# Kernel tuning notes

Measured on AMD Instinct MI355X. Metric: run time of the kernel, lower is better.

The kernel has to match this reference:

```python
import jax, jax.numpy as jnp
import numpy as np

B, S, F, H = 16, 2048, 1024, 16
D = F // H
EPS = 1e-5


def setup_inputs() -> dict:
    key = jax.random.key(0)
    ks = jax.random.split(key, 10)
    scale = 1.0 / np.sqrt(F)
    return {
        "x": jax.random.normal(ks[0], (B, S, F), jnp.float32),
        "Wq": jax.random.normal(ks[1], (F, F), jnp.float32) * scale,
        "bq": jnp.zeros((F,), jnp.float32),
        "Wk": jax.random.normal(ks[2], (F, F), jnp.float32) * scale,
        "bk": jnp.zeros((F,), jnp.float32),
        "Wv": jax.random.normal(ks[3], (F, F), jnp.float32) * scale,
        "bv": jnp.zeros((F,), jnp.float32),
        "Wo": jax.random.normal(ks[4], (F, F), jnp.float32) * scale,
        "bo": jnp.zeros((F,), jnp.float32),
        "gamma": jnp.ones((F,), jnp.float32),
        "beta": jnp.zeros((F,), jnp.float32),
    }


def reference(x, Wq, bq, Wk, bk, Wv, bv, Wo, bo, gamma, beta):
    # x: (B, S, F). Dropout is identity in eval mode.
    b, s, f = x.shape
    q = (x @ Wq + bq).reshape(b, s, H, D)
    k = (x @ Wk + bk).reshape(b, s, H, D)
    v = (x @ Wv + bv).reshape(b, s, H, D)
    # Faithful to source: the einsum (applied to permuted tensors) contracts
    # across HEADS at each sequence position -> scores (B, S, H, H).
    energy = jnp.einsum('bshd,bsgd->bshg', q, k) / (D ** 0.5)
    attn = jax.nn.softmax(energy, axis=-1)  # softmax over key-head axis
    out = jnp.einsum('bshg,bsgd->bshd', attn, v).reshape(b, s, f)
    out = out @ Wo + bo
    # LayerNorm over last dim (eps=1e-5, affine)
    mu = jnp.mean(out, axis=-1, keepdims=True)
    var = jnp.mean((out - mu) ** 2, axis=-1, keepdims=True)
    return (out - mu) * jax.lax.rsqrt(var + EPS) * gamma + beta
```

## Files before the change

kernel.cpp:

```cpp
#include <hip/hip_runtime.h>
#include <hip/hip_bf16.h>
#include <stdint.h>

#define MM   32768
#define FFD  1024
#define NQKV 3072

typedef __bf16 bf16x8 __attribute__((ext_vector_type(8)));
typedef float  f32x4  __attribute__((ext_vector_type(4)));

__device__ __forceinline__ unsigned short f2bf_bits(float f){
  __hip_bfloat16 h = __float2bfloat16(f);
  unsigned short u;
  __builtin_memcpy(&u, &h, 2);
  return u;
}

__device__ __forceinline__ float bf2f(unsigned short u){
  unsigned int w = ((unsigned int)u) << 16;
  float f;
  __builtin_memcpy(&f, &w, 4);
  return f;
}

__device__ __forceinline__ void gld16(const void* g, void* l){
  const unsigned int* gu = (const unsigned int*)g;
  unsigned int* lu = (unsigned int*)l;
  __builtin_amdgcn_global_load_lds(
      (const __attribute__((address_space(1))) unsigned int*)gu,
      (__attribute__((address_space(3))) unsigned int*)lu,
      16, 0, 0);
}

__global__ __launch_bounds__(256) void k_convert_bf16(const float* __restrict__ in,
                                                      unsigned short* __restrict__ out,
                                                      int n4){
  int i = blockIdx.x * 256 + threadIdx.x;
  if (i >= n4) return;
  float4 v = ((const float4*)in)[i];
  ushort4 r;
  r.x = f2bf_bits(v.x); r.y = f2bf_bits(v.y);
  r.z = f2bf_bits(v.z); r.w = f2bf_bits(v.w);
  ((ushort4*)out)[i] = r;
}

__global__ __launch_bounds__(256) void k_transpose_bf16(const float* __restrict__ in,
                                                        unsigned short* __restrict__ out,
                                                        int rows, int cols){
  __shared__ float tile[32][33];
  int bc = blockIdx.x * 32, br = blockIdx.y * 32;
  int tx = threadIdx.x, ty = threadIdx.y;
  #pragma unroll
  for (int j = 0; j < 32; j += 8)
    tile[ty + j][tx] = in[(size_t)(br + ty + j) * cols + bc + tx];
  __syncthreads();
  #pragma unroll
  for (int j = 0; j < 32; j += 8)
    out[(size_t)(bc + ty + j) * rows + br + tx] = f2bf_bits(tile[tx][ty + j]);
}

template <bool BF16OUT>
__global__ __launch_bounds__(256) void k_gemm_bt(
    const unsigned short* __restrict__ A,
    const unsigned short* __restrict__ Bt,
    const float* __restrict__ b0, const float* __restrict__ b1, const float* __restrict__ b2,
    void* __restrict__ Cout, int M, int N, int K)
{
  __shared__ unsigned short As[128 * 32];
  __shared__ unsigned short Bs[128 * 32];

  const int tid  = threadIdx.x;
  const int lane = tid & 63;
  const int wave = tid >> 6;
  const int wr = wave >> 1, wc = wave & 1;
  const int quad = lane >> 4, lrow = lane & 15;

  const long rowBase = (long)blockIdx.y * 128;
  const long colBase = (long)blockIdx.x * 128;

  f32x4 acc[4][4];
  #pragma unroll
  for (int i = 0; i < 4; i++)
    #pragma unroll
    for (int j = 0; j < 4; j++)
      acc[i][j] = (f32x4){0.f, 0.f, 0.f, 0.f};

  const unsigned short* ga = A  + (rowBase + (tid >> 2)) * (long)K + (tid & 3) * 8;
  const unsigned short* gb = Bt + (colBase + (tid >> 2)) * (long)K + (tid & 3) * 8;
  unsigned short* la = As + tid * 8;
  unsigned short* lb = Bs + tid * 8;
  const long rstep = 64L * K;

  const int nk = K >> 5;
  for (int kt = 0; kt < nk; kt++){
    __syncthreads();
    gld16(ga,         la);
    gld16(ga + rstep, la + 2048);
    gld16(gb,         lb);
    gld16(gb + rstep, lb + 2048);
    __syncthreads();

    bf16x8 af[4], bfr[4];
    #pragma unroll
    for (int i = 0; i < 4; i++)
      af[i]  = *(const bf16x8*)(As + (wr * 64 + i * 16 + lrow) * 32 + quad * 8);
    #pragma unroll
    for (int j = 0; j < 4; j++)
      bfr[j] = *(const bf16x8*)(Bs + (wc * 64 + j * 16 + lrow) * 32 + quad * 8);

    #pragma unroll
    for (int i = 0; i < 4; i++)
      #pragma unroll
      for (int j = 0; j < 4; j++)
        acc[i][j] = __builtin_amdgcn_mfma_f32_16x16x32_bf16(af[i], bfr[j], acc[i][j], 0, 0, 0);

    ga += 32; gb += 32;
  }

  #pragma unroll
  for (int j = 0; j < 4; j++){
    long col = colBase + wc * 64 + j * 16 + lrow;
    const float* bp = (col < 1024) ? b0 : ((col < 2048) ? b1 : b2);
    float bias = bp[col & 1023];
    #pragma unroll
    for (int i = 0; i < 4; i++){
      long row0 = rowBase + wr * 64 + i * 16 + quad * 4;
      #pragma unroll
      for (int r = 0; r < 4; r++){
        float v = acc[i][j][r] + bias;
        if constexpr (BF16OUT)
          ((unsigned short*)Cout)[(row0 + r) * (long)N + col] = f2bf_bits(v);
        else
          ((float*)Cout)[(row0 + r) * (long)N + col] = v;
      }
    }
  }
}

__global__ __launch_bounds__(256) void k_attention(const unsigned short* __restrict__ qkv,
                                                   unsigned short* __restrict__ aout){
  constexpr int STRIDE = 68;
  constexpr int MATSZ  = 16 * STRIDE;
  constexpr int PER    = 3 * MATSZ + 16 * 17;
  __shared__ float smem[4 * PER];

  const int lane = threadIdx.x & 63;
  const int wave = threadIdx.x >> 6;
  const int pos  = blockIdx.x * 4 + wave;

  float* base = smem + wave * PER;
  float* qf = base;
  float* kf = base + MATSZ;
  float* vf = base + 2 * MATSZ;
  float* pp = base + 3 * MATSZ;

  const unsigned short* src = qkv + (size_t)pos * 3072;
  #pragma unroll
  for (int i = 0; i < 6; i++){
    int e = (i * 64 + lane) * 8;
    int mat = e >> 10, em = e & 1023;
    int h = em >> 6, d = em & 63;
    uint4 u = *(const uint4*)(src + e);
    const unsigned short* us = (const unsigned short*)&u;
    float* dst = base + mat * MATSZ + h * STRIDE + d;
    #pragma unroll
    for (int t = 0; t < 8; t++) dst[t] = bf2f(us[t]);
  }
  __syncthreads();

  const int h  = lane >> 2;
  const int gq = lane & 3;
  float s[4] = {0.f, 0.f, 0.f, 0.f};
  #pragma unroll
  for (int d4 = 0; d4 < 16; d4++){
    float4 qv = *(const float4*)(qf + h * STRIDE + d4 * 4);
    #pragma unroll
    for (int jj = 0; jj < 4; jj++){
      float4 kv = *(const float4*)(kf + (gq * 4 + jj) * STRIDE + d4 * 4);
      s[jj] += qv.x * kv.x + qv.y * kv.y + qv.z * kv.z + qv.w * kv.w;
    }
  }
  #pragma unroll
  for (int jj = 0; jj < 4; jj++) s[jj] *= 0.125f;

  float m = fmaxf(fmaxf(s[0], s[1]), fmaxf(s[2], s[3]));
  m = fmaxf(m, __shfl_xor(m, 1));
  m = fmaxf(m, __shfl_xor(m, 2));
  float e0 = __expf(s[0] - m), e1 = __expf(s[1] - m);
  float e2 = __expf(s[2] - m), e3 = __expf(s[3] - m);
  float sum = e0 + e1 + e2 + e3;
  sum += __shfl_xor(sum, 1);
  sum += __shfl_xor(sum, 2);
  float inv = 1.0f / sum;
  pp[h * 17 + gq * 4 + 0] = e0 * inv;
  pp[h * 17 + gq * 4 + 1] = e1 * inv;
  pp[h * 17 + gq * 4 + 2] = e2 * inv;
  pp[h * 17 + gq * 4 + 3] = e3 * inv;
  __syncthreads();

  const int dbase = (lane & 3) * 16;
  float4 o0 = {0,0,0,0}, o1 = {0,0,0,0}, o2 = {0,0,0,0}, o3 = {0,0,0,0};
  #pragma unroll
  for (int g = 0; g < 16; g++){
    float p = pp[h * 17 + g];
    const float* vb = vf + g * STRIDE + dbase;
    float4 v0 = *(const float4*)(vb);
    float4 v1 = *(const float4*)(vb + 4);
    float4 v2 = *(const float4*)(vb + 8);
    float4 v3 = *(const float4*)(vb + 12);
    o0.x += p * v0.x; o0.y += p * v0.y; o0.z += p * v0.z; o0.w += p * v0.w;
    o1.x += p * v1.x; o1.y += p * v1.y; o1.z += p * v1.z; o1.w += p * v1.w;
    o2.x += p * v2.x; o2.y += p * v2.y; o2.z += p * v2.z; o2.w += p * v2.w;
    o3.x += p * v3.x; o3.y += p * v3.y; o3.z += p * v3.z; o3.w += p * v3.w;
  }
  unsigned short* dst = aout + (size_t)pos * 1024 + h * 64 + dbase;
  ushort4 r;
  r.x = f2bf_bits(o0.x); r.y = f2bf_bits(o0.y); r.z = f2bf_bits(o0.z); r.w = f2bf_bits(o0.w);
  ((ushort4*)dst)[0] = r;
  r.x = f2bf_bits(o1.x); r.y = f2bf_bits(o1.y); r.z = f2bf_bits(o1.z); r.w = f2bf_bits(o1.w);
  ((ushort4*)dst)[1] = r;
  r.x = f2bf_bits(o2.x); r.y = f2bf_bits(o2.y); r.z = f2bf_bits(o2.z); r.w = f2bf_bits(o2.w);
  ((ushort4*)dst)[2] = r;
  r.x = f2bf_bits(o3.x); r.y = f2bf_bits(o3.y); r.z = f2bf_bits(o3.z); r.w = f2bf_bits(o3.w);
  ((ushort4*)dst)[3] = r;
}

__global__ __launch_bounds__(256) void k_ln(float* __restrict__ out,
                                            const float* __restrict__ gamma,
                                            const float* __restrict__ beta){
  __shared__ float red[8];
  int tid = threadIdx.x;
  float4* rowp = (float4*)(out + (size_t)blockIdx.x * 1024);
  float4 v = rowp[tid];
  float s  = v.x + v.y + v.z + v.w;
  float ss = v.x * v.x + v.y * v.y + v.z * v.z + v.w * v.w;
  #pragma unroll
  for (int off = 32; off > 0; off >>= 1){
    s  += __shfl_down(s, off);
    ss += __shfl_down(ss, off);
  }
  if ((tid & 63) == 0){ red[tid >> 6] = s; red[4 + (tid >> 6)] = ss; }
  __syncthreads();
  float S  = red[0] + red[1] + red[2] + red[3];
  float SS = red[4] + red[5] + red[6] + red[7];
  float mean = S * (1.0f / 1024.0f);
  float var  = SS * (1.0f / 1024.0f) - mean * mean;
  float rstd = rsqrtf(var + 1e-5f);
  float4 g = ((const float4*)gamma)[tid];
  float4 b = ((const float4*)beta)[tid];
  v.x = (v.x - mean) * rstd * g.x + b.x;
  v.y = (v.y - mean) * rstd * g.y + b.y;
  v.z = (v.z - mean) * rstd * g.z + b.z;
  v.w = (v.w - mean) * rstd * g.w + b.w;
  rowp[tid] = v;
}

extern "C" void kernel_launch(void* const* d_in, const int* in_sizes, int n_in,
                              void* d_out, int out_size, void* d_ws, size_t ws_size,
                              hipStream_t stream){
  const float* x     = (const float*)d_in[0];
  const float* Wq    = (const float*)d_in[1];
  const float* bq    = (const float*)d_in[2];
  const float* Wk    = (const float*)d_in[3];
  const float* bk    = (const float*)d_in[4];
  const float* Wv    = (const float*)d_in[5];
  const float* bv    = (const float*)d_in[6];
  const float* Wo    = (const float*)d_in[7];
  const float* bo    = (const float*)d_in[8];
  const float* gamma = (const float*)d_in[9];
  const float* beta  = (const float*)d_in[10];
  float* out = (float*)d_out;

  char* ws = (char*)d_ws;
  unsigned short* Wqkv_t = (unsigned short*)ws;
  unsigned short* Wo_t   = (unsigned short*)(ws + 6291456);
  unsigned short* xb     = (unsigned short*)(ws + 8388608);
  unsigned short* qkv    = (unsigned short*)(ws + 75497472);
  unsigned short* aout   = xb;

  k_convert_bf16<<<32768, 256, 0, stream>>>(x, xb, (MM * FFD) / 4);

  dim3 tb(32, 8), tg(32, 32);
  k_transpose_bf16<<<tg, tb, 0, stream>>>(Wq, Wqkv_t,                1024, 1024);
  k_transpose_bf16<<<tg, tb, 0, stream>>>(Wk, Wqkv_t + 1024 * 1024,  1024, 1024);
  k_transpose_bf16<<<tg, tb, 0, stream>>>(Wv, Wqkv_t + 2048 * 1024,  1024, 1024);
  k_transpose_bf16<<<tg, tb, 0, stream>>>(Wo, Wo_t,                  1024, 1024);

  k_gemm_bt<true><<<dim3(NQKV / 128, MM / 128), 256, 0, stream>>>(
      xb, Wqkv_t, bq, bk, bv, qkv, MM, NQKV, FFD);

  k_attention<<<MM / 4, 256, 0, stream>>>(qkv, aout);

  k_gemm_bt<false><<<dim3(FFD / 128, MM / 128), 256, 0, stream>>>(
      aout, Wo_t, bo, bo, bo, out, MM, FFD, FFD);

  k_ln<<<MM, 256, 0, stream>>>(out, gamma, beta);
}
```

Baseline: 727.8 us.

## Move per-position head attention onto MFMA and double GEMM K-tile depth

```diff
diff --git a/kernel.cpp b/kernel.cpp
--- a/kernel.cpp
+++ b/kernel.cpp
@@ -14,13 +14,6 @@
   unsigned short u;
   __builtin_memcpy(&u, &h, 2);
   return u;
-}
-
-__device__ __forceinline__ float bf2f(unsigned short u){
-  unsigned int w = ((unsigned int)u) << 16;
-  float f;
-  __builtin_memcpy(&f, &w, 4);
-  return f;
 }
 
 __device__ __forceinline__ void gld16(const void* g, void* l){
@@ -66,8 +59,8 @@
     const float* __restrict__ b0, const float* __restrict__ b1, const float* __restrict__ b2,
     void* __restrict__ Cout, int M, int N, int K)
 {
-  __shared__ unsigned short As[128 * 32];
-  __shared__ unsigned short Bs[128 * 32];
+  __shared__ unsigned short As[128 * 64];
+  __shared__ unsigned short Bs[128 * 64];
 
   const int tid  = threadIdx.x;
   const int lane = tid & 63;
@@ -91,30 +84,39 @@
   unsigned short* lb = Bs + tid * 8;
   const long rstep = 64L * K;
 
-  const int nk = K >> 5;
+  const int nk = K >> 6;
   for (int kt = 0; kt < nk; kt++){
     __syncthreads();
-    gld16(ga,         la);
-    gld16(ga + rstep, la + 2048);
-    gld16(gb,         lb);
-    gld16(gb + rstep, lb + 2048);
+    gld16(ga,               la);
+    gld16(ga + rstep,       la + 2048);
+    gld16(ga + 32,          la + 4096);
+    gld16(ga + 32 + rstep,  la + 6144);
+    gld16(gb,               lb);
+    gld16(gb + rstep,       lb + 2048);
+    gld16(gb + 32,          lb + 4096);
+    gld16(gb + 32 + rstep,  lb + 6144);
     __syncthreads();
 
-    bf16x8 af[4], bfr[4];
     #pragma unroll
-    for (int i = 0; i < 4; i++)
-      af[i]  = *(const bf16x8*)(As + (wr * 64 + i * 16 + lrow) * 32 + quad * 8);
-    #pragma unroll
-    for (int j = 0; j < 4; j++)
-      bfr[j] = *(const bf16x8*)(Bs + (wc * 64 + j * 16 + lrow) * 32 + quad * 8);
-
-    #pragma unroll
-    for (int i = 0; i < 4; i++)
+    for (int kk = 0; kk < 2; kk++){
+      const unsigned short* Ah = As + kk * 4096;
+      const unsigned short* Bh = Bs + kk * 4096;
+      bf16x8 af[4], bfr[4];
+      #pragma unroll
+      for (int i = 0; i < 4; i++)
+        af[i]  = *(const bf16x8*)(Ah + (wr * 64 + i * 16 + lrow) * 32 + quad * 8);
       #pragma unroll
       for (int j = 0; j < 4; j++)
-        acc[i][j] = __builtin_amdgcn_mfma_f32_16x16x32_bf16(af[i], bfr[j], acc[i][j], 0, 0, 0);
-
-    ga += 32; gb += 32;
+        bfr[j] = *(const bf16x8*)(Bh + (wc * 64 + j * 16 + lrow) * 32 + quad * 8);
+
+      #pragma unroll
+      for (int i = 0; i < 4; i++)
+        #pragma unroll
+        for (int j = 0; j < 4; j++)
+          acc[i][j] = __builtin_amdgcn_mfma_f32_16x16x32_bf16(af[i], bfr[j], acc[i][j], 0, 0, 0);
+    }
+
+    ga += 64; gb += 64;
   }
 
   #pragma unroll
@@ -139,90 +141,100 @@
 
 __global__ __launch_bounds__(256) void k_attention(const unsigned short* __restrict__ qkv,
                                                    unsigned short* __restrict__ aout){
-  constexpr int STRIDE = 68;
-  constexpr int MATSZ  = 16 * STRIDE;
-  constexpr int PER    = 3 * MATSZ + 16 * 17;
-  __shared__ float smem[4 * PER];
+  constexpr int QOFF = 0;
+  constexpr int KOFF = 1152;
+  constexpr int VOFF = 2304;
+  constexpr int POFF = 4864;
+  constexpr int PER  = 5504;
+  __shared__ unsigned short smem[4 * PER];
 
   const int lane = threadIdx.x & 63;
   const int wave = threadIdx.x >> 6;
   const int pos  = blockIdx.x * 4 + wave;
-
-  float* base = smem + wave * PER;
-  float* qf = base;
-  float* kf = base + MATSZ;
-  float* vf = base + 2 * MATSZ;
-  float* pp = base + 3 * MATSZ;
+  const int quad = lane >> 4, lidx = lane & 15;
+
+  unsigned short* base = smem + wave * PER;
+  unsigned short* Qb = base + QOFF;
+  unsigned short* Kb = base + KOFF;
+  unsigned short* Vt = base + VOFF;
+  unsigned short* Pb = base + POFF;
+
+  {
+    uint4 z = {0u, 0u, 0u, 0u};
+    *(uint4*)(Vt + lane * 40 + 16) = z;
+    *(uint4*)(Vt + lane * 40 + 24) = z;
+    *(uint2*)(Pb + (lane >> 2) * 40 + 16 + (lane & 3) * 4) = make_uint2(0u, 0u);
+  }
 
   const unsigned short* src = qkv + (size_t)pos * 3072;
   #pragma unroll
   for (int i = 0; i < 6; i++){
-    int e = (i * 64 + lane) * 8;
-    int mat = e >> 10, em = e & 1023;
-    int h = em >> 6, d = em & 63;
-    uint4 u = *(const uint4*)(src + e);
-    const unsigned short* us = (const unsigned short*)&u;
-    float* dst = base + mat * MATSZ + h * STRIDE + d;
+    int c = i * 64 + lane;
+    uint4 u = *(const uint4*)(src + c * 8);
+    if (i < 4){
+      unsigned short* mb = (c < 128) ? Qb : Kb;
+      int cc = c & 127;
+      *(uint4*)(mb + (cc >> 3) * 72 + (cc & 7) * 8) = u;
+    } else {
+      int cv = c - 256;
+      int g = cv >> 3, d0 = (cv & 7) * 8;
+      const unsigned short* us = (const unsigned short*)&u;
+      #pragma unroll
+      for (int t = 0; t < 8; t++) Vt[(d0 + t) * 40 + g] = us[t];
+    }
+  }
+  __syncthreads();
+
+  f32x4 s = (f32x4){0.f, 0.f, 0.f, 0.f};
+  #pragma unroll
+  for (int kk = 0; kk < 2; kk++){
+    bf16x8 a = *(const bf16x8*)(Qb + lidx * 72 + kk * 32 + quad * 8);
+    bf16x8 b = *(const bf16x8*)(Kb + lidx * 72 + kk * 32 + quad * 8);
+    s = __builtin_amdgcn_mfma_f32_16x16x32_bf16(a, b, s, 0, 0, 0);
+  }
+
+  #pragma unroll
+  for (int r = 0; r < 4; r++){
+    float v = s[r] * 0.125f;
+    float m = v;
+    m = fmaxf(m, __shfl_xor(m, 1));
+    m = fmaxf(m, __shfl_xor(m, 2));
+    m = fmaxf(m, __shfl_xor(m, 4));
+    m = fmaxf(m, __shfl_xor(m, 8));
+    float e = __expf(v - m);
+    float sum = e;
+    sum += __shfl_xor(sum, 1);
+    sum += __shfl_xor(sum, 2);
+    sum += __shfl_xor(sum, 4);
+    sum += __shfl_xor(sum, 8);
+    float p = e / sum;
+    Pb[(quad * 4 + r) * 40 + lidx] = f2bf_bits(p);
+  }
+  __syncthreads();
+
+  f32x4 o[4];
+  #pragma unroll
+  for (int n4 = 0; n4 < 4; n4++){
+    bf16x8 a = *(const bf16x8*)(Pb + lidx * 40 + quad * 8);
+    bf16x8 b = *(const bf16x8*)(Vt + (n4 * 16 + lidx) * 40 + quad * 8);
+    o[n4] = __builtin_amdgcn_mfma_f32_16x16x32_bf16(a, b, (f32x4){0.f,0.f,0.f,0.f}, 0, 0, 0);
+  }
+
+  #pragma unroll
+  for (int n4 = 0; n4 < 4; n4++)
     #pragma unroll
-    for (int t = 0; t < 8; t++) dst[t] = bf2f(us[t]);
-  }
-  __syncthreads();
-
-  const int h  = lane >> 2;
-  const int gq = lane & 3;
-  float s[4] = {0.f, 0.f, 0.f, 0.f};
-  #pragma unroll
-  for (int d4 = 0; d4 < 16; d4++){
-    float4 qv = *(const float4*)(qf + h * STRIDE + d4 * 4);
-    #pragma unroll
-    for (int jj = 0; jj < 4; jj++){
-      float4 kv = *(const float4*)(kf + (gq * 4 + jj) * STRIDE + d4 * 4);
-      s[jj] += qv.x * kv.x + qv.y * kv.y + qv.z * kv.z + qv.w * kv.w;
-    }
-  }
-  #pragma unroll
-  for (int jj = 0; jj < 4; jj++) s[jj] *= 0.125f;
-
-  float m = fmaxf(fmaxf(s[0], s[1]), fmaxf(s[2], s[3]));
-  m = fmaxf(m, __shfl_xor(m, 1));
-  m = fmaxf(m, __shfl_xor(m, 2));
-  float e0 = __expf(s[0] - m), e1 = __expf(s[1] - m);
-  float e2 = __expf(s[2] - m), e3 = __expf(s[3] - m);
-  float sum = e0 + e1 + e2 + e3;
-  sum += __shfl_xor(sum, 1);
-  sum += __shfl_xor(sum, 2);
-  float inv = 1.0f / sum;
-  pp[h * 17 + gq * 4 + 0] = e0 * inv;
-  pp[h * 17 + gq * 4 + 1] = e1 * inv;
-  pp[h * 17 + gq * 4 + 2] = e2 * inv;
-  pp[h * 17 + gq * 4 + 3] = e3 * inv;
-  __syncthreads();
-
-  const int dbase = (lane & 3) * 16;
-  float4 o0 = {0,0,0,0}, o1 = {0,0,0,0}, o2 = {0,0,0,0}, o3 = {0,0,0,0};
-  #pragma unroll
-  for (int g = 0; g < 16; g++){
-    float p = pp[h * 17 + g];
-    const float* vb = vf + g * STRIDE + dbase;
-    float4 v0 = *(const float4*)(vb);
-    float4 v1 = *(const float4*)(vb + 4);
-    float4 v2 = *(const float4*)(vb + 8);
-    float4 v3 = *(const float4*)(vb + 12);
-    o0.x += p * v0.x; o0.y += p * v0.y; o0.z += p * v0.z; o0.w += p * v0.w;
-    o1.x += p * v1.x; o1.y += p * v1.y; o1.z += p * v1.z; o1.w += p * v1.w;
-    o2.x += p * v2.x; o2.y += p * v2.y; o2.z += p * v2.z; o2.w += p * v2.w;
-    o3.x += p * v3.x; o3.y += p * v3.y; o3.z += p * v3.z; o3.w += p * v3.w;
-  }
-  unsigned short* dst = aout + (size_t)pos * 1024 + h * 64 + dbase;
-  ushort4 r;
-  r.x = f2bf_bits(o0.x); r.y = f2bf_bits(o0.y); r.z = f2bf_bits(o0.z); r.w = f2bf_bits(o0.w);
-  ((ushort4*)dst)[0] = r;
-  r.x = f2bf_bits(o1.x); r.y = f2bf_bits(o1.y); r.z = f2bf_bits(o1.z); r.w = f2bf_bits(o1.w);
-  ((ushort4*)dst)[1] = r;
-  r.x = f2bf_bits(o2.x); r.y = f2bf_bits(o2.y); r.z = f2bf_bits(o2.z); r.w = f2bf_bits(o2.w);
-  ((ushort4*)dst)[2] = r;
-  r.x = f2bf_bits(o3.x); r.y = f2bf_bits(o3.y); r.z = f2bf_bits(o3.z); r.w = f2bf_bits(o3.w);
-  ((ushort4*)dst)[3] = r;
+    for (int r = 0; r < 4; r++)
+      Qb[(quad * 4 + r) * 72 + n4 * 16 + lidx] = f2bf_bits(o[n4][r]);
+  __syncthreads();
+
+  unsigned short* dst = aout + (size_t)pos * 1024;
+  #pragma unroll
+  for (int t = 0; t < 2; t++){
+    int j = lane * 2 + t;
+    int h = j >> 3, dc = j & 7;
+    uint4 u = *(const uint4*)(Qb + h * 72 + dc * 8);
+    *(uint4*)(dst + j * 8) = u;
+  }
 }
 
 __global__ __launch_bounds__(256) void k_ln(float* __restrict__ out,
```

Result: faster. 704.1 us (-3.3%).
